# Optimization experiments

Hardware: AMD Instinct MI355X
Metric: run time of the kernel (lower is better)

## Reference

```python
import jax, jax.numpy as jnp
import numpy as np

B, N0, N, CP, CS, C1, C2 = 8, 8192, 2048, 512, 256, 256, 256
BN_EPS = 1e-3
SLOPE = 0.01


def setup_inputs() -> dict:
    key = jax.random.key(0)
    ks = jax.random.split(key, 10)
    xyz = jax.random.normal(ks[0], (B, 3, N0), jnp.float32)
    skip = jax.random.normal(ks[1], (B, CS, N0), jnp.float32)
    xyz_prev = jax.random.normal(ks[2], (B, 3, N), jnp.float32)
    feat_prev = jax.random.normal(ks[3], (B, CP, N), jnp.float32)
    W1 = jax.random.normal(ks[4], (C1, CP + CS), jnp.float32) * 0.05
    g1 = jax.random.uniform(ks[5], (C1,), jnp.float32, 0.5, 1.5)
    b1 = jax.random.normal(ks[6], (C1,), jnp.float32) * 0.1
    W2 = jax.random.normal(ks[7], (C2, C1), jnp.float32) * 0.05
    g2 = jax.random.uniform(ks[8], (C2,), jnp.float32, 0.5, 1.5)
    b2 = jax.random.normal(ks[9], (C2,), jnp.float32) * 0.1
    return dict(xyz=xyz, skip=skip, xyz_prev=xyz_prev, feat_prev=feat_prev,
                W1=W1, g1=g1, b1=b1, W2=W2, g2=g2, b2=b2)


def _three_interp(xyz, xyz_prev, feat_prev):
    # xyz: [B,3,N0] query points; xyz_prev: [B,3,N] source; feat_prev: [B,CP,N]
    x = xyz.transpose(0, 2, 1)        # [B,N0,3]
    y = xyz_prev.transpose(0, 2, 1)   # [B,N,3]
    d2 = ((x * x).sum(-1)[:, :, None] + (y * y).sum(-1)[:, None, :]
          - 2.0 * jnp.einsum('bnd,bmd->bnm', x, y))   # [B,N0,N] squared dists
    neg_vals, idx = jax.lax.top_k(-d2, 3)             # 3 smallest distances
    d2nn = jnp.maximum(-neg_vals, 1e-10)              # dist*dist with clamp
    inv = 1.0 / (d2nn + 1e-8)
    w = inv / inv.sum(-1, keepdims=True)              # [B,N0,3]
    # gather feat_prev[b,c,idx[b,n,k]] -> [B,CP,N0,3]
    gathered = jnp.take_along_axis(feat_prev[:, :, None, :], idx[:, None, :, :], axis=3)
    return (gathered * w[:, None, :, :]).sum(-1)      # [B,CP,N0]


def _conv_bn_lrelu(x, W, g, b):
    # conv1x1 (no bias) + BatchNorm1d (training-mode batch stats, eps=1e-3) + LeakyReLU(0.01)
    y = jnp.einsum('oc,bcn->bon', W, x)
    mean = y.mean(axis=(0, 2), keepdims=True)
    var = ((y - mean) ** 2).mean(axis=(0, 2), keepdims=True)
    y = (y - mean) * jax.lax.rsqrt(var + BN_EPS) * g[None, :, None] + b[None, :, None]
    return jnp.where(y >= 0, y, SLOPE * y)


def reference(xyz, skip, xyz_prev, feat_prev, W1, g1, b1, W2, g2, b2):
    nf = _three_interp(xyz, xyz_prev, feat_prev)      # [B,CP,N0]
    nf = jnp.concatenate([nf, skip], axis=1)          # [B,CP+CS,N0]
    nf = _conv_bn_lrelu(nf, W1, g1, b1)
    nf = _conv_bn_lrelu(nf, W2, g2, b2)
    return xyz, nf
```

## Files before the change

### kernel.cpp

```cpp
#include <hip/hip_runtime.h>
#include <hip/hip_bf16.h>

using bf16 = __hip_bfloat16;

constexpr int B  = 8;
constexpr int N0 = 8192;
constexpr int NS = 2048;
constexpr int CP = 512;
constexpr int CS = 256;
constexpr int C1 = 256;
constexpr int C2 = 256;
constexpr int K1 = CP + CS;
constexpr int COLS = B * N0;
constexpr float BN_EPS = 1e-3f;
constexpr float SLOPE  = 0.01f;

typedef short  short8 __attribute__((ext_vector_type(8)));
typedef float  f32x4  __attribute__((ext_vector_type(4)));

typedef __attribute__((address_space(1))) unsigned int gas_uint;
typedef __attribute__((address_space(3))) unsigned int las_uint;

#define BARX() do { asm volatile("" ::: "memory"); __builtin_amdgcn_s_barrier(); asm volatile("" ::: "memory"); } while (0)
#define VM12()  asm volatile("s_waitcnt vmcnt(12)" ::: "memory")
#define VM0()   asm volatile("s_waitcnt vmcnt(0)"  ::: "memory")
#define LGKM0() asm volatile("s_waitcnt lgkmcnt(0)" ::: "memory")

__device__ __forceinline__ unsigned short f2bu(float f) {
  unsigned int u = __float_as_uint(f);
  return (unsigned short)((u + 0x7fffu + ((u >> 16) & 1u)) >> 16);
}
__device__ __forceinline__ float bu2f(unsigned short v) {
  return __uint_as_float((unsigned int)v << 16);
}

__global__ __launch_bounds__(256) void prep_kernel(
    const float* __restrict__ W1, const float* __restrict__ W2,
    unsigned short* __restrict__ W1b, unsigned short* __restrict__ W2b,
    float* __restrict__ stats)
{
  int id = blockIdx.x * 256 + threadIdx.x;
  if (id < 1024) stats[id] = 0.0f;
  if (id < C1 * K1) W1b[id] = f2bu(W1[id]);
  if (id < C2 * C1) W2b[id] = f2bu(W2[id]);
}

__global__ __launch_bounds__(256) void knn_kernel(
    const float* __restrict__ xyz, const float* __restrict__ xyz_prev,
    float* __restrict__ wq, int* __restrict__ iq)
{
#pragma clang fp contract(off)
  __shared__ float4 sp[NS];
  __shared__ float  md[4][64][3];
  __shared__ int    mi[4][64][3];
  const int b = blockIdx.y;
  const float* xp = xyz_prev + (size_t)b * 3 * NS;
  for (int j = threadIdx.x; j < NS; j += 256) {
    float x = xp[j], y = xp[NS + j], z = xp[2 * NS + j];
    sp[j] = make_float4(x, y, z, (x * x + y * y) + z * z);
  }
  __syncthreads();

  const int q  = threadIdx.x & 63;
  const int sl = threadIdx.x >> 6;
  const int n  = blockIdx.x * 64 + q;
  const float* xq = xyz + (size_t)b * 3 * N0;
  float qx = xq[n], qy = xq[N0 + n], qz = xq[2 * N0 + n];
  float qq = (qx * qx + qy * qy) + qz * qz;

  const int j0 = sl * (NS / 4);
  float a0 = 1e30f, a1 = 1e30f, a2 = 1e30f;
  int   ai0 = 0, ai1 = 0, ai2 = 0;
  float c0 = 1e30f, c1 = 1e30f, c2 = 1e30f;
  int   ci0 = 0, ci1 = 0, ci2 = 0;
#pragma unroll 2
  for (int jj = 0; jj < NS / 8; ++jj) {
    const int ja = j0 + jj, jc = j0 + NS / 8 + jj;
    float4 pa = sp[ja];
    float4 pc = sp[jc];
    float dota = (qx * pa.x + qy * pa.y) + qz * pa.z;
    float da = (qq + pa.w) - 2.0f * dota;
    float dotc = (qx * pc.x + qy * pc.y) + qz * pc.z;
    float dc = (qq + pc.w) - 2.0f * dotc;
    if (da < a0)      { a2 = a1; ai2 = ai1; a1 = a0; ai1 = ai0; a0 = da; ai0 = ja; }
    else if (da < a1) { a2 = a1; ai2 = ai1; a1 = da; ai1 = ja; }
    else if (da < a2) { a2 = da; ai2 = ja; }
    if (dc < c0)      { c2 = c1; ci2 = ci1; c1 = c0; ci1 = ci0; c0 = dc; ci0 = jc; }
    else if (dc < c1) { c2 = c1; ci2 = ci1; c1 = dc; ci1 = jc; }
    else if (dc < c2) { c2 = dc; ci2 = jc; }
  }
  {
    float dv[3] = {c0, c1, c2}; int iv[3] = {ci0, ci1, ci2};
#pragma unroll
    for (int t = 0; t < 3; ++t) {
      float d = dv[t]; int ii = iv[t];
      if (d < a0)      { a2 = a1; ai2 = ai1; a1 = a0; ai1 = ai0; a0 = d; ai0 = ii; }
      else if (d < a1) { a2 = a1; ai2 = ai1; a1 = d;  ai1 = ii; }
      else if (d < a2) { a2 = d;  ai2 = ii; }
    }
  }
  md[sl][q][0] = a0; md[sl][q][1] = a1; md[sl][q][2] = a2;
  mi[sl][q][0] = ai0; mi[sl][q][1] = ai1; mi[sl][q][2] = ai2;
  __syncthreads();

  if (threadIdx.x < 64) {
    float e0 = 1e30f, e1 = 1e30f, e2 = 1e30f;
    int   k0 = 0, k1 = 0, k2 = 0;
#pragma unroll
    for (int s = 0; s < 4; ++s) {
#pragma unroll
      for (int t = 0; t < 3; ++t) {
        float d = md[s][q][t]; int ii = mi[s][q][t];
        if (d < e0)      { e2 = e1; k2 = k1; e1 = e0; k1 = k0; e0 = d; k0 = ii; }
        else if (d < e1) { e2 = e1; k2 = k1; e1 = d;  k1 = ii; }
        else if (d < e2) { e2 = d;  k2 = ii; }
      }
    }
    e0 = fmaxf(e0, 1e-10f); e1 = fmaxf(e1, 1e-10f); e2 = fmaxf(e2, 1e-10f);
    float v0 = 1.0f / (e0 + 1e-8f), v1 = 1.0f / (e1 + 1e-8f), v2 = 1.0f / (e2 + 1e-8f);
    float s = (v0 + v1) + v2;
    const int gi = (b * N0 + n) * 3;
    wq[gi + 0] = v0 / s; wq[gi + 1] = v1 / s; wq[gi + 2] = v2 / s;
    iq[gi + 0] = k0;     iq[gi + 1] = k1;     iq[gi + 2] = k2;
  }
}

__global__ __launch_bounds__(256) void interp_kernel(
    const float* __restrict__ feat_prev, const int* __restrict__ iq,
    const float* __restrict__ wq, unsigned short* __restrict__ Xt)
{
  __shared__ unsigned short sf[16 * 2048];
  const int bx = blockIdx.x;
  const int b  = bx >> 6;
  const int cg = (bx >> 1) & 31;
  const int nh = bx & 1;
  const int c0 = cg * 16;
  const float* fp = feat_prev + ((size_t)b * CP + c0) * NS;

  for (int id = threadIdx.x; id < 8192; id += 256) {
    float4 v = reinterpret_cast<const float4*>(fp)[id];
    ushort4 o;
    o.x = f2bu(v.x); o.y = f2bu(v.y); o.z = f2bu(v.z); o.w = f2bu(v.w);
    *reinterpret_cast<ushort4*>(&sf[id * 4]) = o;
  }
  __syncthreads();

  const int nbase = nh * 4096;
  for (int it = 0; it < 16; ++it) {
    const int n    = nbase + it * 256 + threadIdx.x;
    const int gcol = b * N0 + n;
    const int gq   = gcol * 3;
    const int i0 = iq[gq], i1 = iq[gq + 1], i2 = iq[gq + 2];
    const float w0 = wq[gq], w1 = wq[gq + 1], w2 = wq[gq + 2];
    unsigned short outv[16];
#pragma unroll
    for (int c = 0; c < 16; ++c) {
      const unsigned short* row = &sf[c * 2048];
      float v = w0 * bu2f(row[i0]) + w1 * bu2f(row[i1]) + w2 * bu2f(row[i2]);
      outv[c] = f2bu(v);
    }
    unsigned short* dst = Xt + (size_t)gcol * K1 + c0;
    *reinterpret_cast<short8*>(dst)     = *reinterpret_cast<short8*>(&outv[0]);
    *reinterpret_cast<short8*>(dst + 8) = *reinterpret_cast<short8*>(&outv[8]);
  }
}

__global__ __launch_bounds__(256) void skipt_kernel(
    const float* __restrict__ skip, unsigned short* __restrict__ Xt)
{
  __shared__ float T[64][65];
  const int kt   = blockIdx.x & 3;
  const int ct   = blockIdx.x >> 2;
  const int col0 = ct * 64;
  const int b    = col0 >> 13;
  const int n0   = col0 & 8191;
  const float* src = skip + ((size_t)b * CS + kt * 64) * N0 + n0;

  for (int id = threadIdx.x; id < 1024; id += 256) {
    int r = id >> 4, q = id & 15;
    float4 v = *reinterpret_cast<const float4*>(src + (size_t)r * N0 + q * 4);
    T[r][q * 4 + 0] = v.x; T[r][q * 4 + 1] = v.y;
    T[r][q * 4 + 2] = v.z; T[r][q * 4 + 3] = v.w;
  }
  __syncthreads();
  for (int id = threadIdx.x; id < 512; id += 256) {
    int n = id >> 3, q = id & 7;
    alignas(16) unsigned short tmp[8];
#pragma unroll
    for (int j = 0; j < 8; ++j) tmp[j] = f2bu(T[q * 8 + j][n]);
    *reinterpret_cast<short8*>(Xt + (size_t)(col0 + n) * K1 + CP + kt * 64 + q * 8) =
        *reinterpret_cast<short8*>(tmp);
  }
}

__global__ __launch_bounds__(256, 2) void gemm1_kernel(
    const unsigned short* __restrict__ W1b, const unsigned short* __restrict__ Xt,
    unsigned short* __restrict__ Y1t, float* __restrict__ stats)
{
  __shared__ unsigned short Bs[2][128 * 64];
  __shared__ unsigned short scr[64][264];

  const int tid   = threadIdx.x;
  const int gcol0 = blockIdx.x * 128;

  const int wv = tid >> 6, lane = tid & 63;
  const int wm = wv * 64;
  const int qm = lane & 15, quad = lane >> 4;
  const int lr = lane >> 3, lc = lane & 7;
  const int sw_src = (lc ^ lr) * 8;
  const int sw_rd  = qm & 7;

  f32x4 acc[4][8];
#pragma unroll
  for (int i = 0; i < 4; ++i)
#pragma unroll
    for (int j = 0; j < 8; ++j) acc[i][j] = (f32x4){0.f, 0.f, 0.f, 0.f};

  auto stageB = [&](int kt, int buf) {
    const int kof = kt * 64 + sw_src;
#pragma unroll
    for (int t = 0; t < 4; ++t) {
      const int ch = wv * 4 + t;
      const int r  = ch * 8 + lr;
      __builtin_amdgcn_global_load_lds(
          (const gas_uint*)(Xt + (size_t)(gcol0 + r) * K1 + kof),
          (las_uint*)(&Bs[buf][ch * 512]), 16, 0, 0);
    }
  };
  auto loadA = [&](int kt, short8 (&af)[2][4]) {
#pragma unroll
    for (int h = 0; h < 2; ++h)
#pragma unroll
      for (int i = 0; i < 4; ++i)
        af[h][i] = *reinterpret_cast<const short8*>(
            W1b + (size_t)(wm + i * 16 + qm) * K1 + kt * 64 + h * 32 + quad * 8);
  };
  auto compute = [&](const short8 (&af)[2][4], int buf) {
    const unsigned short* Bb = &Bs[buf][0];
#pragma unroll
    for (int h = 0; h < 2; ++h) {
      short8 bf[8];
#pragma unroll
      for (int j = 0; j < 8; ++j)
        bf[j] = *reinterpret_cast<const short8*>(
            &Bb[(j * 16 + qm) * 64 + ((h * 4 + quad) ^ sw_rd) * 8]);
#pragma unroll
      for (int i = 0; i < 4; ++i)
#pragma unroll
        for (int j = 0; j < 8; ++j)
          acc[i][j] = __builtin_amdgcn_mfma_f32_16x16x32_bf16(af[h][i], bf[j], acc[i][j], 0, 0, 0);
    }
  };

  short8 afA[2][4], afB[2][4];
  stageB(0, 0); loadA(0, afA);
  stageB(1, 1); loadA(1, afB);

  for (int kt = 0; kt < K1 / 64; kt += 2) {
    VM12();
    BARX();
    compute(afA, 0);
    BARX();
    if (kt + 2 < K1 / 64) { stageB(kt + 2, 0); loadA(kt + 2, afA); }
    if (kt < 10) { VM12(); } else { VM0(); }
    BARX();
    compute(afB, 1);
    BARX();
    if (kt + 3 < K1 / 64) { stageB(kt + 3, 1); loadA(kt + 3, afB); }
  }

#pragma unroll
  for (int i = 0; i < 4; ++i) {
    const int mb = wm + i * 16 + quad * 4;
    float s[4] = {0.f, 0.f, 0.f, 0.f}, s2[4] = {0.f, 0.f, 0.f, 0.f};
#pragma unroll
    for (int j = 0; j < 8; ++j) {
#pragma unroll
      for (int r = 0; r < 4; ++r) {
        float v = acc[i][j][r];
        s[r] += v; s2[r] += v * v;
      }
    }
#pragma unroll
    for (int m = 1; m < 16; m <<= 1) {
#pragma unroll
      for (int r = 0; r < 4; ++r) { s[r] += __shfl_xor(s[r], m); s2[r] += __shfl_xor(s2[r], m); }
    }
    if (qm == 0) {
#pragma unroll
      for (int r = 0; r < 4; ++r) {
        atomicAdd(&stats[mb + r], s[r]);
        atomicAdd(&stats[C1 + mb + r], s2[r]);
      }
    }
  }

#pragma unroll
  for (int half = 0; half < 2; ++half) {
#pragma unroll
    for (int i = 0; i < 4; ++i) {
      const int mb = wm + i * 16 + quad * 4;
#pragma unroll
      for (int jj = 0; jj < 4; ++jj) {
        const int j = half * 4 + jj;
        ushort4 o;
        o.x = f2bu(acc[i][j][0]); o.y = f2bu(acc[i][j][1]);
        o.z = f2bu(acc[i][j][2]); o.w = f2bu(acc[i][j][3]);
        *reinterpret_cast<ushort4*>(&scr[jj * 16 + qm][mb]) = o;
      }
    }
    LGKM0();
    BARX();
#pragma unroll
    for (int u = 0; u < 8; ++u) {
      const int flat = tid * 16 + u * 4096;
      const int r = flat >> 9, c = (flat & 511) >> 1;
      short8 v = *reinterpret_cast<const short8*>(&scr[r][c]);
      *reinterpret_cast<short8*>(Y1t + (((size_t)(gcol0 + half * 64 + r)) << 8) + c) = v;
    }
    if (half == 0) BARX();
  }
}

__global__ __launch_bounds__(256) void affine_kernel(
    const float* __restrict__ s, const float* __restrict__ g,
    const float* __restrict__ bb, float* __restrict__ a)
{
  int c = threadIdx.x;
  float inv = 1.0f / (float)COLS;
  float mean = s[c] * inv;
  float var  = s[C1 + c] * inv - mean * mean;
  float sc   = g[c] / sqrtf(var + BN_EPS);
  a[c]      = sc;
  a[C1 + c] = bb[c] - mean * sc;
}

__global__ __launch_bounds__(256, 2) void gemm2_kernel(
    const unsigned short* __restrict__ W2b, const unsigned short* __restrict__ Y1t,
    const float* __restrict__ aff, float* __restrict__ out_nf,
    float* __restrict__ stats2)
{
  __shared__ unsigned short Bs[2][128][72];

  const int tid   = threadIdx.x;
  const int gcol0 = blockIdx.x * 128;
  const int b     = gcol0 >> 13;
  const int ncol0 = gcol0 & 8191;

  const int wv = tid >> 6, lane = tid & 63;
  const int wm = wv * 64;
  const int qm = lane & 15, quad = lane >> 4;
  const int sn = tid >> 1;
  const int sck = (tid & 1) * 4;

  f32x4 acc[4][8];
#pragma unroll
  for (int i = 0; i < 4; ++i)
#pragma unroll
    for (int j = 0; j < 8; ++j) acc[i][j] = (f32x4){0.f, 0.f, 0.f, 0.f};

  short8 afA[2][4], afB[2][4];
  short8 bregA[4], bregB[4];

  auto loadA = [&](int kt, short8 (&af)[2][4]) {
#pragma unroll
    for (int h = 0; h < 2; ++h)
#pragma unroll
      for (int i = 0; i < 4; ++i)
        af[h][i] = *reinterpret_cast<const short8*>(
            W2b + (size_t)(wm + i * 16 + qm) * C1 + kt * 64 + h * 32 + quad * 8);
  };
  auto loadB = [&](int kt, short8 (&breg)[4]) {
#pragma unroll
    for (int t = 0; t < 4; ++t)
      breg[t] = *reinterpret_cast<const short8*>(
          Y1t + (size_t)(gcol0 + sn) * C1 + kt * 64 + (sck + t) * 8);
  };
  auto xformWrite = [&](const short8 (&breg)[4], int kt, int buf) {
#pragma unroll
    for (int t = 0; t < 4; ++t) {
      const int c0 = kt * 64 + (sck + t) * 8;
      float4 sc0 = *reinterpret_cast<const float4*>(aff + c0);
      float4 sc1 = *reinterpret_cast<const float4*>(aff + c0 + 4);
      float4 sh0 = *reinterpret_cast<const float4*>(aff + C1 + c0);
      float4 sh1 = *reinterpret_cast<const float4*>(aff + C1 + c0 + 4);
      alignas(16) unsigned short tmp[8];
#pragma unroll
      for (int j = 0; j < 4; ++j) {
        float v = bu2f((unsigned short)breg[t][j]) * (&sc0.x)[j] + (&sh0.x)[j];
        v = (v >= 0.f) ? v : SLOPE * v;
        tmp[j] = f2bu(v);
      }
#pragma unroll
      for (int j = 0; j < 4; ++j) {
        float v = bu2f((unsigned short)breg[t][4 + j]) * (&sc1.x)[j] + (&sh1.x)[j];
        v = (v >= 0.f) ? v : SLOPE * v;
        tmp[4 + j] = f2bu(v);
      }
      *reinterpret_cast<short8*>(&Bs[buf][sn][(sck + t) * 8]) =
          *reinterpret_cast<short8*>(tmp);
    }
  };
  auto compute = [&](const short8 (&af)[2][4], int buf) {
#pragma unroll
    for (int h = 0; h < 2; ++h) {
      short8 bf[8];
#pragma unroll
      for (int j = 0; j < 8; ++j)
        bf[j] = *reinterpret_cast<const short8*>(
            &Bs[buf][j * 16 + qm][(h * 4 + quad) * 8]);
#pragma unroll
      for (int i = 0; i < 4; ++i)
#pragma unroll
        for (int j = 0; j < 8; ++j)
          acc[i][j] = __builtin_amdgcn_mfma_f32_16x16x32_bf16(af[h][i], bf[j], acc[i][j], 0, 0, 0);
    }
  };

  loadB(0, bregA); loadA(0, afA);
  loadB(1, bregB); loadA(1, afB);
  xformWrite(bregA, 0, 0);
  LGKM0(); BARX();
  compute(afA, 0);
  xformWrite(bregB, 1, 1);
  loadB(2, bregA); loadA(2, afA);
  LGKM0(); BARX();
  compute(afB, 1);
  xformWrite(bregA, 2, 0);
  loadB(3, bregB); loadA(3, afB);
  LGKM0(); BARX();
  compute(afA, 0);
  xformWrite(bregB, 3, 1);
  LGKM0(); BARX();
  compute(afB, 1);

#pragma unroll
  for (int i = 0; i < 4; ++i) {
    const int mb = wm + i * 16 + quad * 4;
    float s[4] = {0.f, 0.f, 0.f, 0.f}, s2[4] = {0.f, 0.f, 0.f, 0.f};
#pragma unroll
    for (int j = 0; j < 8; ++j) {
      const int col = ncol0 + j * 16 + qm;
#pragma unroll
      for (int r = 0; r < 4; ++r) {
        float v = acc[i][j][r];
        out_nf[((size_t)b * C2 + mb + r) * N0 + col] = v;
        s[r] += v; s2[r] += v * v;
      }
    }
#pragma unroll
    for (int m = 1; m < 16; m <<= 1) {
#pragma unroll
      for (int r = 0; r < 4; ++r) { s[r] += __shfl_xor(s[r], m); s2[r] += __shfl_xor(s2[r], m); }
    }
    if (qm == 0) {
#pragma unroll
      for (int r = 0; r < 4; ++r) {
        atomicAdd(&stats2[mb + r], s[r]);
        atomicAdd(&stats2[C2 + mb + r], s2[r]);
      }
    }
  }
}

__global__ __launch_bounds__(256) void finalize_kernel(float* __restrict__ nf,
                                                       const float* __restrict__ aff)
{
  int id4 = blockIdx.x * 256 + threadIdx.x;
  int e = id4 * 4;
  int c = (e % (C2 * N0)) / N0;
  float sc = aff[c], sh = aff[C1 + c];
  float4 v = reinterpret_cast<float4*>(nf)[id4];
  v.x = v.x * sc + sh; v.x = (v.x >= 0.f) ? v.x : SLOPE * v.x;
  v.y = v.y * sc + sh; v.y = (v.y >= 0.f) ? v.y : SLOPE * v.y;
  v.z = v.z * sc + sh; v.z = (v.z >= 0.f) ? v.z : SLOPE * v.z;
  v.w = v.w * sc + sh; v.w = (v.w >= 0.f) ? v.w : SLOPE * v.w;
  reinterpret_cast<float4*>(nf)[id4] = v;
}

__global__ __launch_bounds__(256) void copy_xyz_kernel(const float* __restrict__ xyz,
                                                       float* __restrict__ out)
{
  int id = blockIdx.x * 256 + threadIdx.x;
  reinterpret_cast<float4*>(out)[id] = reinterpret_cast<const float4*>(xyz)[id];
}

extern "C" void kernel_launch(void* const* d_in, const int* in_sizes, int n_in,
                              void* d_out, int out_size, void* d_ws, size_t ws_size,
                              hipStream_t stream)
{
  const float* xyz       = (const float*)d_in[0];
  const float* skip      = (const float*)d_in[1];
  const float* xyz_prev  = (const float*)d_in[2];
  const float* feat_prev = (const float*)d_in[3];
  const float* W1        = (const float*)d_in[4];
  const float* g1        = (const float*)d_in[5];
  const float* b1        = (const float*)d_in[6];
  const float* W2        = (const float*)d_in[7];
  const float* g2        = (const float*)d_in[8];
  const float* b2        = (const float*)d_in[9];

  float* out    = (float*)d_out;
  float* out_nf = out + (size_t)B * 3 * N0;

  char* ws = (char*)d_ws;
  float*          wq    = (float*)(ws + 0);
  int*            iq    = (int*)  (ws + 786432);
  unsigned short* W1b   = (unsigned short*)(ws + 1572864);
  unsigned short* W2b   = (unsigned short*)(ws + 1966080);
  float*          stats = (float*)(ws + 2097152);
  float*          aff   = (float*)(ws + 2101248);
  unsigned short* Y1t   = (unsigned short*)(ws + 2105344);
  unsigned short* Xt    = (unsigned short*)(ws + 35659776);

  prep_kernel<<<768, 256, 0, stream>>>(W1, W2, W1b, W2b, stats);
  knn_kernel<<<dim3(N0 / 64, B), 256, 0, stream>>>(xyz, xyz_prev, wq, iq);
  interp_kernel<<<512, 256, 0, stream>>>(feat_prev, iq, wq, Xt);
  skipt_kernel<<<4096, 256, 0, stream>>>(skip, Xt);
  gemm1_kernel<<<COLS / 128, 256, 0, stream>>>(W1b, Xt, Y1t, stats);
  affine_kernel<<<1, 256, 0, stream>>>(stats, g1, b1, aff);
  gemm2_kernel<<<COLS / 128, 256, 0, stream>>>(W2b, Y1t, aff, out_nf, stats + 512);
  affine_kernel<<<1, 256, 0, stream>>>(stats + 512, g2, b2, aff + 512);
  finalize_kernel<<<(C2 * N0 * B) / (4 * 256), 256, 0, stream>>>(out_nf, aff + 512);
  copy_xyz_kernel<<<(B * 3 * N0) / (4 * 256), 256, 0, stream>>>(xyz, out);
}
```

Baseline: 494.3 us.

## Split GEMM tiles across eight waves with 2D warp layout, direct Y1 stores

Both GEMM kernels now launch 512 threads per block and give each wave a 64x64 sub-tile in a 4x2 arrangement, halving per-wave accumulators and B-fragment loads. gemm1 drops the LDS scratch transpose and writes bf16 results straight to global memory. It also restructures the prefetch so A-fragments load one stage later, with vmcnt waits adjusted to match. The aim is more waves in flight to hide latency and lower register pressure. The trade-offs are the launch bound of one block per CU, each A-fragment now loaded by two waves, and narrower, less coalesced output stores.

```diff
diff --git a/kernel.cpp b/kernel.cpp
--- a/kernel.cpp
+++ b/kernel.cpp
@@ -22,7 +22,7 @@
 typedef __attribute__((address_space(3))) unsigned int las_uint;
 
 #define BARX() do { asm volatile("" ::: "memory"); __builtin_amdgcn_s_barrier(); asm volatile("" ::: "memory"); } while (0)
-#define VM12()  asm volatile("s_waitcnt vmcnt(12)" ::: "memory")
+#define VM2()   asm volatile("s_waitcnt vmcnt(2)"  ::: "memory")
 #define VM0()   asm volatile("s_waitcnt vmcnt(0)"  ::: "memory")
 #define LGKM0() asm volatile("s_waitcnt lgkmcnt(0)" ::: "memory")
 
@@ -193,34 +193,34 @@
   }
 }
 
-__global__ __launch_bounds__(256, 2) void gemm1_kernel(
+__global__ __launch_bounds__(512, 1) void gemm1_kernel(
     const unsigned short* __restrict__ W1b, const unsigned short* __restrict__ Xt,
     unsigned short* __restrict__ Y1t, float* __restrict__ stats)
 {
   __shared__ unsigned short Bs[2][128 * 64];
-  __shared__ unsigned short scr[64][264];
 
   const int tid   = threadIdx.x;
   const int gcol0 = blockIdx.x * 128;
 
   const int wv = tid >> 6, lane = tid & 63;
-  const int wm = wv * 64;
+  const int wm = (wv >> 1) * 64;
+  const int wn = (wv & 1) * 64;
   const int qm = lane & 15, quad = lane >> 4;
   const int lr = lane >> 3, lc = lane & 7;
   const int sw_src = (lc ^ lr) * 8;
   const int sw_rd  = qm & 7;
 
-  f32x4 acc[4][8];
+  f32x4 acc[4][4];
 #pragma unroll
   for (int i = 0; i < 4; ++i)
 #pragma unroll
-    for (int j = 0; j < 8; ++j) acc[i][j] = (f32x4){0.f, 0.f, 0.f, 0.f};
+    for (int j = 0; j < 4; ++j) acc[i][j] = (f32x4){0.f, 0.f, 0.f, 0.f};
 
   auto stageB = [&](int kt, int buf) {
     const int kof = kt * 64 + sw_src;
 #pragma unroll
-    for (int t = 0; t < 4; ++t) {
-      const int ch = wv * 4 + t;
+    for (int t = 0; t < 2; ++t) {
+      const int ch = wv * 2 + t;
       const int r  = ch * 8 + lr;
       __builtin_amdgcn_global_load_lds(
           (const gas_uint*)(Xt + (size_t)(gcol0 + r) * K1 + kof),
@@ -239,34 +239,35 @@
     const unsigned short* Bb = &Bs[buf][0];
 #pragma unroll
     for (int h = 0; h < 2; ++h) {
-      short8 bf[8];
-#pragma unroll
-      for (int j = 0; j < 8; ++j)
+      short8 bf[4];
+#pragma unroll
+      for (int j = 0; j < 4; ++j)
         bf[j] = *reinterpret_cast<const short8*>(
-            &Bb[(j * 16 + qm) * 64 + ((h * 4 + quad) ^ sw_rd) * 8]);
+            &Bb[(wn + j * 16 + qm) * 64 + ((h * 4 + quad) ^ sw_rd) * 8]);
 #pragma unroll
       for (int i = 0; i < 4; ++i)
 #pragma unroll
-        for (int j = 0; j < 8; ++j)
+        for (int j = 0; j < 4; ++j)
           acc[i][j] = __builtin_amdgcn_mfma_f32_16x16x32_bf16(af[h][i], bf[j], acc[i][j], 0, 0, 0);
     }
   };
 
   short8 afA[2][4], afB[2][4];
-  stageB(0, 0); loadA(0, afA);
-  stageB(1, 1); loadA(1, afB);
+  stageB(0, 0); loadA(0, afA); stageB(1, 1);
 
   for (int kt = 0; kt < K1 / 64; kt += 2) {
-    VM12();
+    VM2();
     BARX();
+    if (kt + 1 < K1 / 64) loadA(kt + 1, afB);
     compute(afA, 0);
     BARX();
-    if (kt + 2 < K1 / 64) { stageB(kt + 2, 0); loadA(kt + 2, afA); }
-    if (kt < 10) { VM12(); } else { VM0(); }
+    if (kt + 2 < K1 / 64) stageB(kt + 2, 0);
+    if (kt + 3 < K1 / 64) { VM2(); } else { VM0(); }
     BARX();
+    if (kt + 2 < K1 / 64) loadA(kt + 2, afA);
     compute(afB, 1);
     BARX();
-    if (kt + 3 < K1 / 64) { stageB(kt + 3, 1); loadA(kt + 3, afB); }
+    if (kt + 3 < K1 / 64) stageB(kt + 3, 1);
   }
 
 #pragma unroll
@@ -274,7 +275,12 @@
     const int mb = wm + i * 16 + quad * 4;
     float s[4] = {0.f, 0.f, 0.f, 0.f}, s2[4] = {0.f, 0.f, 0.f, 0.f};
 #pragma unroll
-    for (int j = 0; j < 8; ++j) {
+    for (int j = 0; j < 4; ++j) {
+      const int gc = gcol0 + wn + j * 16 + qm;
+      ushort4 o;
+      o.x = f2bu(acc[i][j][0]); o.y = f2bu(acc[i][j][1]);
+      o.z = f2bu(acc[i][j][2]); o.w = f2bu(acc[i][j][3]);
+      *reinterpret_cast<ushort4*>(Y1t + (size_t)gc * C1 + mb) = o;
 #pragma unroll
       for (int r = 0; r < 4; ++r) {
         float v = acc[i][j][r];
@@ -293,32 +299,6 @@
         atomicAdd(&stats[C1 + mb + r], s2[r]);
       }
     }
-  }
-
-#pragma unroll
-  for (int half = 0; half < 2; ++half) {
-#pragma unroll
-    for (int i = 0; i < 4; ++i) {
-      const int mb = wm + i * 16 + quad * 4;
-#pragma unroll
-      for (int jj = 0; jj < 4; ++jj) {
-        const int j = half * 4 + jj;
-        ushort4 o;
-        o.x = f2bu(acc[i][j][0]); o.y = f2bu(acc[i][j][1]);
-        o.z = f2bu(acc[i][j][2]); o.w = f2bu(acc[i][j][3]);
-        *reinterpret_cast<ushort4*>(&scr[jj * 16 + qm][mb]) = o;
-      }
-    }
-    LGKM0();
-    BARX();
-#pragma unroll
-    for (int u = 0; u < 8; ++u) {
-      const int flat = tid * 16 + u * 4096;
-      const int r = flat >> 9, c = (flat & 511) >> 1;
-      short8 v = *reinterpret_cast<const short8*>(&scr[r][c]);
-      *reinterpret_cast<short8*>(Y1t + (((size_t)(gcol0 + half * 64 + r)) << 8) + c) = v;
-    }
-    if (half == 0) BARX();
   }
 }
 
@@ -335,7 +315,7 @@
   a[C1 + c] = bb[c] - mean * sc;
 }
 
-__global__ __launch_bounds__(256, 2) void gemm2_kernel(
+__global__ __launch_bounds__(512, 1) void gemm2_kernel(
     const unsigned short* __restrict__ W2b, const unsigned short* __restrict__ Y1t,
     const float* __restrict__ aff, float* __restrict__ out_nf,
     float* __restrict__ stats2)
@@ -348,19 +328,20 @@
   const int ncol0 = gcol0 & 8191;
 
   const int wv = tid >> 6, lane = tid & 63;
-  const int wm = wv * 64;
+  const int wm = (wv >> 1) * 64;
+  const int wn = (wv & 1) * 64;
   const int qm = lane & 15, quad = lane >> 4;
-  const int sn = tid >> 1;
-  const int sck = (tid & 1) * 4;
-
-  f32x4 acc[4][8];
+  const int sn = tid >> 2;
+  const int sck = (tid & 3) * 2;
+
+  f32x4 acc[4][4];
 #pragma unroll
   for (int i = 0; i < 4; ++i)
 #pragma unroll
-    for (int j = 0; j < 8; ++j) acc[i][j] = (f32x4){0.f, 0.f, 0.f, 0.f};
+    for (int j = 0; j < 4; ++j) acc[i][j] = (f32x4){0.f, 0.f, 0.f, 0.f};
 
   short8 afA[2][4], afB[2][4];
-  short8 bregA[4], bregB[4];
+  short8 bregA[2], bregB[2];
 
   auto loadA = [&](int kt, short8 (&af)[2][4]) {
 #pragma unroll
@@ -370,15 +351,15 @@
         af[h][i] = *reinterpret_cast<const short8*>(
             W2b + (size_t)(wm + i * 16 + qm) * C1 + kt * 64 + h * 32 + quad * 8);
   };
-  auto loadB = [&](int kt, short8 (&breg)[4]) {
-#pragma unroll
-    for (int t = 0; t < 4; ++t)
+  auto loadB = [&](int kt, short8 (&breg)[2]) {
+#pragma unroll
+    for (int t = 0; t < 2; ++t)
       breg[t] = *reinterpret_cast<const short8*>(
           Y1t + (size_t)(gcol0 + sn) * C1 + kt * 64 + (sck + t) * 8);
   };
-  auto xformWrite = [&](const short8 (&breg)[4], int kt, int buf) {
-#pragma unroll
-    for (int t = 0; t < 4; ++t) {
+  auto xformWrite = [&](const short8 (&breg)[2], int kt, int buf) {
+#pragma unroll
+    for (int t = 0; t < 2; ++t) {
       const int c0 = kt * 64 + (sck + t) * 8;
       float4 sc0 = *reinterpret_cast<const float4*>(aff + c0);
       float4 sc1 = *reinterpret_cast<const float4*>(aff + c0 + 4);
@@ -404,15 +385,15 @@
   auto compute = [&](const short8 (&af)[2][4], int buf) {
 #pragma unroll
     for (int h = 0; h < 2; ++h) {
-      short8 bf[8];
-#pragma unroll
-      for (int j = 0; j < 8; ++j)
+      short8 bf[4];
+#pragma unroll
+      for (int j = 0; j < 4; ++j)
         bf[j] = *reinterpret_cast<const short8*>(
-            &Bs[buf][j * 16 + qm][(h * 4 + quad) * 8]);
+            &Bs[buf][wn + j * 16 + qm][(h * 4 + quad) * 8]);
 #pragma unroll
       for (int i = 0; i < 4; ++i)
 #pragma unroll
-        for (int j = 0; j < 8; ++j)
+        for (int j = 0; j < 4; ++j)
           acc[i][j] = __builtin_amdgcn_mfma_f32_16x16x32_bf16(af[h][i], bf[j], acc[i][j], 0, 0, 0);
     }
   };
@@ -439,8 +420,8 @@
     const int mb = wm + i * 16 + quad * 4;
     float s[4] = {0.f, 0.f, 0.f, 0.f}, s2[4] = {0.f, 0.f, 0.f, 0.f};
 #pragma unroll
-    for (int j = 0; j < 8; ++j) {
-      const int col = ncol0 + j * 16 + qm;
+    for (int j = 0; j < 4; ++j) {
+      const int col = ncol0 + wn + j * 16 + qm;
 #pragma unroll
       for (int r = 0; r < 4; ++r) {
         float v = acc[i][j][r];
@@ -517,9 +498,9 @@
   knn_kernel<<<dim3(N0 / 64, B), 256, 0, stream>>>(xyz, xyz_prev, wq, iq);
   interp_kernel<<<512, 256, 0, stream>>>(feat_prev, iq, wq, Xt);
   skipt_kernel<<<4096, 256, 0, stream>>>(skip, Xt);
-  gemm1_kernel<<<COLS / 128, 256, 0, stream>>>(W1b, Xt, Y1t, stats);
+  gemm1_kernel<<<COLS / 128, 512, 0, stream>>>(W1b, Xt, Y1t, stats);
   affine_kernel<<<1, 256, 0, stream>>>(stats, g1, b1, aff);
-  gemm2_kernel<<<COLS / 128, 256, 0, stream>>>(W2b, Y1t, aff, out_nf, stats + 512);
+  gemm2_kernel<<<COLS / 128, 512, 0, stream>>>(W2b, Y1t, aff, out_nf, stats + 512);
   affine_kernel<<<1, 256, 0, stream>>>(stats + 512, g2, b2, aff + 512);
   finalize_kernel<<<(C2 * N0 * B) / (4 * 256), 256, 0, stream>>>(out_nf, aff + 512);
   copy_xyz_kernel<<<(B * 3 * N0) / (4 * 256), 256, 0, stream>>>(xyz, out);
```

Result: slower. 626.3 us (+26.7%).
